# Kernel tuning notes

Hardware: AMD Instinct MI355X
Metric: run time of the kernel (lower is better)

## Reference

```python
import jax, jax.numpy as jnp
import numpy as np

ALPHA = 1.0          # gating temperature (train_alpha=False)
DEPTH = 4            # floor(log2(leaves=16))
LEAF_NUM = 16        # 2**DEPTH
N_INTERNAL = LEAF_NUM - 2  # nodes 1..14 (root handled separately)
B, D, OUT = 8192, 512, 64


def _prob(x, pw, aW, ab):
    # vectorized Node.prob with set_comps=True (comparators recomputed from batch mean)
    comp = -jnp.mean(x * pw, axis=0)                      # [in]
    dist = jax.nn.sigmoid(ALPHA * (pw * x + comp))        # [B, in]
    attn = jax.nn.softmax(x @ aW.T + ab, axis=-1)         # [B, in]
    return jnp.sum(dist * attn, axis=1, keepdims=True)    # [B, 1]


def setup_inputs() -> dict:
    key = jax.random.key(0)
    ks = jax.random.split(key, 12)
    s = 0.02
    return {
        "x": jax.random.normal(ks[0], (B, D), jnp.float32),
        # root node (input_size=D, output_size=D)
        "calc_W0": jax.random.normal(ks[1], (D, D), jnp.float32) * s,
        "calc_b0": jnp.zeros((D,), jnp.float32),
        "prob_w0": jax.random.uniform(ks[2], (D,), jnp.float32),
        "attn_W0": jax.random.normal(ks[3], (D, D), jnp.float32) * s,
        "attn_b0": jnp.zeros((D,), jnp.float32),
        # internal nodes 1..14 (input_size=2D, output_size=D), stacked
        "calc_W": jax.random.normal(ks[4], (N_INTERNAL, D, 2 * D), jnp.float32) * s,
        "calc_b": jnp.zeros((N_INTERNAL, D), jnp.float32),
        "prob_w": jax.random.uniform(ks[5], (N_INTERNAL, 2 * D), jnp.float32),
        "attn_W": jax.random.normal(ks[6], (N_INTERNAL, 2 * D, 2 * D), jnp.float32) * s,
        "attn_b": jnp.zeros((N_INTERNAL, 2 * D), jnp.float32),
        # leaf nodes: learned output vectors (torch.rand init)
        "leaf_out": jax.random.uniform(ks[7], (LEAF_NUM, OUT), jnp.float32),
    }


def reference(x, calc_W0, calc_b0, prob_w0, attn_W0, attn_b0,
              calc_W, calc_b, prob_w, attn_W, attn_b, leaf_out):
    outs, probab = {}, {}
    # root
    outs[0] = jax.nn.relu(x @ calc_W0.T + calc_b0)            # [B, D]
    p = _prob(x, prob_w0, attn_W0, attn_b0)                   # [B, 1]
    probab[1] = 1.0 - p
    probab[2] = p
    # internal nodes 1..leaf_num-2 (binary-tree routing)
    for n in range(1, LEAF_NUM - 1):
        parent = (n - 1) // 2
        inp = jnp.concatenate([outs[parent], x], axis=1)      # [B, 2D]
        outs[n] = jax.nn.relu(inp @ calc_W[n - 1].T + calc_b[n - 1])
        p = _prob(inp, prob_w[n - 1], attn_W[n - 1], attn_b[n - 1])
        probab[2 * n + 1] = probab[n] * (1.0 - p)
        probab[2 * n + 2] = probab[n] * p
    # leaves: indices LEAF_NUM-1 .. 2*LEAF_NUM-2
    leaf_p = jnp.concatenate([probab[i + LEAF_NUM - 1] for i in range(LEAF_NUM)], axis=1)  # [B, 16]
    # sum over leaves of probab * leaf_out == leaf_p @ leaf_out
    actions = leaf_p @ leaf_out                                # [B, OUT]
    return jax.nn.softmax(actions, axis=-1)
```

## Files before the change

### kernel.cpp

```cpp
#include <hip/hip_runtime.h>
#include <hip/hip_bf16.h>
#include <cstdint>


#define NROWS 8192
#define HALFD 512

typedef __bf16 bf16x8 __attribute__((ext_vector_type(8)));
typedef short  short8 __attribute__((ext_vector_type(8)));
typedef float  f32x4  __attribute__((ext_vector_type(4)));

union FragU { short8 s; bf16x8 b; };

struct GArgs {
  const __hip_bfloat16* A0[4];
  const __hip_bfloat16* Bw[4];
  const float* bias[4];
  const float* pw[4];
  const float* cm0[4];
  __hip_bfloat16* outB[4];
  float* csOut[4];
  float* S1[4];
  float* S2[4];
  int mode[4];
  int gx[4];
  int K[4];
};

__device__ __forceinline__ void gl2lds16(const void* g, void* l) {
  __builtin_amdgcn_global_load_lds((__attribute__((address_space(1))) void*)g,
                                   (__attribute__((address_space(3))) void*)l,
                                   16, 0, 0);
}

struct CvtArgs { const float* src[5]; __hip_bfloat16* dst[5]; int nblk[5]; };
__global__ void k_cvt(CvtArgs a) {
  int b = blockIdx.x, r = 0;
  while (b >= a.nblk[r]) { b -= a.nblk[r]; ++r; }
  const int i = (b * 256 + threadIdx.x) * 4;
  float4 v = *(const float4*)(a.src[r] + i);
  union { short4 s4; __hip_bfloat16 h[4]; } u;
  u.h[0] = __float2bfloat16(v.x);
  u.h[1] = __float2bfloat16(v.y);
  u.h[2] = __float2bfloat16(v.z);
  u.h[3] = __float2bfloat16(v.w);
  *(short4*)(a.dst[r] + i) = u.s4;
}

__global__ void k_colsum_f32(const float* __restrict__ src, float* __restrict__ dst) {
  int c  = blockIdx.x * 256 + threadIdx.x;
  int r0 = blockIdx.y * 256;
  float s = 0.f;
  for (int r = 0; r < 256; ++r) s += src[(size_t)(r0 + r) * HALFD + c];
  atomicAdd(&dst[c], s);
}

__global__ __launch_bounds__(256, 2)
void k_gemm(GArgs ga, const __hip_bfloat16* __restrict__ A1,
            const float* __restrict__ cm1) {
  __shared__ alignas(16) short As[128 * 64];
  __shared__ alignas(16) short Bs[128 * 64];

  const int z = blockIdx.z;
  const int id  = blockIdx.x + gridDim.x * blockIdx.y;
  const int xcd = id & 7;
  const int q   = id >> 3;
  const int bx  = q >> 3;
  const int by  = xcd * 8 + (q & 7);
  if (bx >= ga.gx[z]) return;

  const __hip_bfloat16* __restrict__ Ah0 = ga.A0[z];
  const __hip_bfloat16* __restrict__ Bw  = ga.Bw[z];
  const float* __restrict__ bias = ga.bias[z];
  const int K = ga.K[z];

  const int tid  = threadIdx.x;
  const int lane = tid & 63;
  const int wv   = tid >> 6;
  const int wm   = wv >> 1, wn = wv & 1;
  const int lr   = lane & 15, lg = lane >> 4;
  const int row0 = by * 128;
  const int col0 = bx * 128;

  f32x4 acc[4][4];
#pragma unroll
  for (int i = 0; i < 4; ++i)
#pragma unroll
    for (int j = 0; j < 4; ++j)
#pragma unroll
      for (int e = 0; e < 4; ++e) acc[i][j][e] = 0.f;

  const int sr = tid >> 3;
  const int sc = (((tid & 7) ^ (sr & 7)) << 3);
  const int sw = lr & 7;

  for (int kt = 0; kt < K; kt += 64) {
    const __hip_bfloat16* Asrc = (kt < HALFD) ? Ah0 : A1;
    const int kl = kt & (HALFD - 1);
    __syncthreads();
#pragma unroll
    for (int rnd = 0; rnd < 4; ++rnd) {
      const int r = rnd * 32 + sr;
      gl2lds16(Asrc + (size_t)(row0 + r) * HALFD + kl + sc,
               (char*)As + rnd * 4096 + wv * 1024);
      gl2lds16(Bw + (size_t)(col0 + r) * K + kt + sc,
               (char*)Bs + rnd * 4096 + wv * 1024);
    }
    __syncthreads();
#pragma unroll
    for (int kk = 0; kk < 64; kk += 32) {
      FragU a[4], b[4];
#pragma unroll
      for (int mi = 0; mi < 4; ++mi)
        a[mi].s = *(const short8*)(As + (wm * 64 + mi * 16 + lr) * 64 +
                                   ((((kk >> 3) + lg) ^ sw) << 3));
#pragma unroll
      for (int ni = 0; ni < 4; ++ni)
        b[ni].s = *(const short8*)(Bs + (wn * 64 + ni * 16 + lr) * 64 +
                                   ((((kk >> 3) + lg) ^ sw) << 3));
#pragma unroll
      for (int mi = 0; mi < 4; ++mi)
#pragma unroll
        for (int ni = 0; ni < 4; ++ni)
          acc[mi][ni] = __builtin_amdgcn_mfma_f32_16x16x32_bf16(a[mi].b, b[ni].b,
                                                               acc[mi][ni], 0, 0, 0);
    }
  }

  if (ga.mode[z] == 0) {
    __hip_bfloat16* outB = ga.outB[z];
    float* csOut = ga.csOut[z];
#pragma unroll
    for (int ni = 0; ni < 4; ++ni) {
      const int col  = col0 + wn * 64 + ni * 16 + lr;
      const float bv = bias[col];
      __hip_bfloat16* op = outB + (size_t)(col >> 9) * ((size_t)NROWS * HALFD) + (col & 511);
      float csum = 0.f;
#pragma unroll
      for (int mi = 0; mi < 4; ++mi) {
#pragma unroll
        for (int rg = 0; rg < 4; ++rg) {
          const int row = row0 + wm * 64 + mi * 16 + lg * 4 + rg;
          float v = acc[mi][ni][rg] + bv;
          v = v > 0.f ? v : 0.f;
          csum += v;
          op[(size_t)row * HALFD] = __float2bfloat16(v);
        }
      }
      csum += __shfl_xor(csum, 16);
      csum += __shfl_xor(csum, 32);
      if (lg == 0) atomicAdd(&csOut[col], csum);
    }
  } else {
    const float* __restrict__ pw  = ga.pw[z];
    const float* __restrict__ cm0 = ga.cm0[z];
    const int node  = col0 >> 10;
    const int slice = ((bx & 7) << 1) | wn;
    float* s1p = ga.S1[z] + (size_t)(node * 16 + slice) * NROWS;
    float* s2p = ga.S2[z] + (size_t)(node * 16 + slice) * NROWS;
    float bv[4], pwv[4], cmv[4];
    const __hip_bfloat16* Ain[4];
#pragma unroll
    for (int ni = 0; ni < 4; ++ni) {
      const int col = col0 + wn * 64 + ni * 16 + lr;
      bv[ni]  = bias[col];
      pwv[ni] = pw[col];
      const int ii   = col & 1023;
      const int half = ii >> 9;
      const int cc   = ii & 511;
      cmv[ni] = (half ? cm1[cc] : cm0[cc]) * (1.f / 8192.f);
      Ain[ni] = (half ? A1 : Ah0) + cc;
    }
#pragma unroll
    for (int mi = 0; mi < 4; ++mi) {
#pragma unroll
      for (int rg = 0; rg < 4; ++rg) {
        const int row = row0 + wm * 64 + mi * 16 + lg * 4 + rg;
        float s1 = 0.f, s2 = 0.f;
#pragma unroll
        for (int ni = 0; ni < 4; ++ni) {
          const float l = acc[mi][ni][rg] + bv[ni];
          const float e = __expf(l);
          const float inpv = __bfloat162float(Ain[ni][(size_t)row * HALFD]);
          const float zz = pwv[ni] * (inpv - cmv[ni]);
          const float dist = 1.f / (1.f + __expf(-zz));
          s1 += e;
          s2 += dist * e;
        }
#pragma unroll
        for (int off = 1; off < 16; off <<= 1) {
          s1 += __shfl_xor(s1, off);
          s2 += __shfl_xor(s2, off);
        }
        if (lr == 0) {
          s1p[row] = s1;
          s2p[row] = s2;
        }
      }
    }
  }
}

__global__ void k_finalize(const float* __restrict__ S1, const float* __restrict__ S2,
                           const float* __restrict__ leaf_out, float* __restrict__ out) {
  const int r    = (blockIdx.x * 256 + threadIdx.x) >> 6;
  const int lane = threadIdx.x & 63;
  float pb[31];
  pb[0] = 1.f;
#pragma unroll
  for (int n = 0; n < 15; ++n) {
    float a1 = 0.f, a2 = 0.f;
#pragma unroll
    for (int s = 0; s < 16; ++s) {
      a1 += S1[((size_t)n * 16 + s) * NROWS + r];
      a2 += S2[((size_t)n * 16 + s) * NROWS + r];
    }
    const float p = a2 / a1;
    pb[2 * n + 1] = pb[n] * (1.f - p);
    pb[2 * n + 2] = pb[n] * p;
  }
  float a = 0.f;
#pragma unroll
  for (int i = 0; i < 16; ++i) a += pb[15 + i] * leaf_out[i * 64 + lane];
  float m = a;
#pragma unroll
  for (int off = 1; off < 64; off <<= 1) m = fmaxf(m, __shfl_xor(m, off));
  const float e = __expf(a - m);
  float s = e;
#pragma unroll
  for (int off = 1; off < 64; off <<= 1) s += __shfl_xor(s, off);
  out[(size_t)r * 64 + lane] = e / s;
}

static constexpr size_t O_S1   = 0;
static constexpr size_t O_S2   = O_S1 + (size_t)15 * 16 * NROWS * 4;
static constexpr size_t O_XSUM = O_S2 + (size_t)15 * 16 * NROWS * 4;
static constexpr size_t O_CS   = O_XSUM + 512 * 4;
static constexpr size_t O_ZEND = O_CS + 7 * 512 * 4;
static constexpr size_t O_XB   = O_ZEND;
static constexpr size_t O_OUTS = O_XB + (size_t)NROWS * HALFD * 2;
static constexpr size_t O_CW0  = O_OUTS + 7 * (size_t)NROWS * HALFD * 2;
static constexpr size_t O_AW0  = O_CW0 + (size_t)512 * 512 * 2;
static constexpr size_t O_CW   = O_AW0 + (size_t)512 * 512 * 2;
static constexpr size_t O_AW   = O_CW + (size_t)14 * 512 * 1024 * 2;

extern "C" void kernel_launch(void* const* d_in, const int* in_sizes, int n_in,
                              void* d_out, int out_size, void* d_ws, size_t ws_size,
                              hipStream_t stream) {
  const float* x        = (const float*)d_in[0];
  const float* calc_b0  = (const float*)d_in[2];
  const float* prob_w0  = (const float*)d_in[3];
  const float* attn_b0  = (const float*)d_in[5];
  const float* calc_b   = (const float*)d_in[7];
  const float* prob_w   = (const float*)d_in[8];
  const float* attn_b   = (const float*)d_in[10];
  const float* leaf_out = (const float*)d_in[11];
  float* out = (float*)d_out;
  char* ws = (char*)d_ws;

  float* S1   = (float*)(ws + O_S1);
  float* S2   = (float*)(ws + O_S2);
  float* xsum = (float*)(ws + O_XSUM);
  float* cs   = (float*)(ws + O_CS);
  __hip_bfloat16* xb   = (__hip_bfloat16*)(ws + O_XB);
  __hip_bfloat16* outs = (__hip_bfloat16*)(ws + O_OUTS);
  __hip_bfloat16* cW0b = (__hip_bfloat16*)(ws + O_CW0);
  __hip_bfloat16* aW0b = (__hip_bfloat16*)(ws + O_AW0);
  __hip_bfloat16* cWb  = (__hip_bfloat16*)(ws + O_CW);
  __hip_bfloat16* aWb  = (__hip_bfloat16*)(ws + O_AW);
  const size_t OSZ = (size_t)NROWS * HALFD;
  const size_t NSL = (size_t)16 * NROWS;

  hipMemsetAsync(S1, 0, NSL * 4, stream);
  hipMemsetAsync(S2, 0, NSL * 4, stream);
  hipMemsetAsync(ws + O_XSUM, 0, O_ZEND - O_XSUM, stream);

  {
    CvtArgs ca{};
    ca.src[0] = x;                     ca.dst[0] = xb;   ca.nblk[0] = NROWS * HALFD / 1024;
    ca.src[1] = (const float*)d_in[1]; ca.dst[1] = cW0b; ca.nblk[1] = 512 * 512 / 1024;
    ca.src[2] = (const float*)d_in[4]; ca.dst[2] = aW0b; ca.nblk[2] = 512 * 512 / 1024;
    ca.src[3] = (const float*)d_in[6]; ca.dst[3] = cWb;  ca.nblk[3] = 14 * 512 * 1024 / 1024;
    ca.src[4] = (const float*)d_in[9]; ca.dst[4] = aWb;  ca.nblk[4] = 14 * 1024 * 1024 / 1024;
    int tot = ca.nblk[0] + ca.nblk[1] + ca.nblk[2] + ca.nblk[3] + ca.nblk[4];
    k_cvt<<<tot, 256, 0, stream>>>(ca);
  }
  k_colsum_f32<<<dim3(2, 32), 256, 0, stream>>>(x, xsum);

  {
    GArgs ga{};
    ga.mode[0] = 0; ga.gx[0] = 4; ga.K[0] = 512;
    ga.A0[0] = xb; ga.Bw[0] = cW0b; ga.bias[0] = calc_b0;
    ga.outB[0] = outs; ga.csOut[0] = cs;
    ga.mode[1] = 1; ga.gx[1] = 4; ga.K[1] = 512;
    ga.A0[1] = xb; ga.Bw[1] = aW0b; ga.bias[1] = attn_b0;
    ga.pw[1] = prob_w0; ga.cm0[1] = xsum;
    ga.S1[1] = S1; ga.S2[1] = S2;
    k_gemm<<<dim3(4, 64, 2), 256, 0, stream>>>(ga, xb, xsum);
  }
  {
    GArgs ga{};
    ga.mode[0] = 0; ga.gx[0] = 8; ga.K[0] = 1024;
    ga.A0[0] = outs; ga.Bw[0] = cWb; ga.bias[0] = calc_b;
    ga.outB[0] = outs + OSZ; ga.csOut[0] = cs + 512;
    ga.mode[1] = 1; ga.gx[1] = 16; ga.K[1] = 1024;
    ga.A0[1] = outs; ga.Bw[1] = aWb; ga.bias[1] = attn_b;
    ga.pw[1] = prob_w; ga.cm0[1] = cs;
    ga.S1[1] = S1 + (size_t)1 * NSL; ga.S2[1] = S2 + (size_t)1 * NSL;
    k_gemm<<<dim3(16, 64, 2), 256, 0, stream>>>(ga, xb, xsum);
  }
  {
    GArgs ga{};
    for (int i = 0; i < 2; ++i) {
      ga.mode[i] = 0; ga.gx[i] = 8; ga.K[i] = 1024;
      ga.A0[i] = outs + (size_t)(1 + i) * OSZ;
      ga.Bw[i] = cWb + (size_t)(2 + 2 * i) * 512 * 1024;
      ga.bias[i] = calc_b + (2 + 2 * i) * 512;
      ga.outB[i] = outs + (size_t)(3 + 2 * i) * OSZ;
      ga.csOut[i] = cs + (size_t)(3 + 2 * i) * 512;
    }
    for (int i = 0; i < 2; ++i) {
      const int zi = 2 + i;
      ga.mode[zi] = 1; ga.gx[zi] = 16; ga.K[zi] = 1024;
      ga.A0[zi] = outs + (size_t)(1 + i) * OSZ;
      ga.Bw[zi] = aWb + (size_t)(2 + 2 * i) * 1024 * 1024;
      ga.bias[zi] = attn_b + (2 + 2 * i) * 1024;
      ga.pw[zi] = prob_w + (2 + 2 * i) * 1024;
      ga.cm0[zi] = cs + (size_t)(1 + i) * 512;
      ga.S1[zi] = S1 + (size_t)(3 + 2 * i) * NSL;
      ga.S2[zi] = S2 + (size_t)(3 + 2 * i) * NSL;
    }
    k_gemm<<<dim3(16, 64, 4), 256, 0, stream>>>(ga, xb, xsum);
  }
  {
    GArgs ga{};
    for (int i = 0; i < 4; ++i) {
      ga.mode[i] = 1; ga.gx[i] = 16; ga.K[i] = 1024;
      ga.A0[i] = outs + (size_t)(3 + i) * OSZ;
      ga.Bw[i] = aWb + (size_t)(6 + 2 * i) * 1024 * 1024;
      ga.bias[i] = attn_b + (6 + 2 * i) * 1024;
      ga.pw[i] = prob_w + (6 + 2 * i) * 1024;
      ga.cm0[i] = cs + (size_t)(3 + i) * 512;
      ga.S1[i] = S1 + (size_t)(7 + 2 * i) * NSL;
      ga.S2[i] = S2 + (size_t)(7 + 2 * i) * NSL;
    }
    k_gemm<<<dim3(16, 64, 4), 256, 0, stream>>>(ga, xb, xsum);
  }

  k_finalize<<<NROWS * 64 / 256, 256, 0, stream>>>(S1, S2, leaf_out, out);
}
```

Measured before the change: 593.8 us.

## Double-buffer GEMM shared-memory tiles with prefetch two stages ahead

Converts the GEMM main loop to a two-buffer LDS pipeline. Tiles for steps t+1 and t+2 are issued with direct global-to-LDS loads while step t's MFMAs run, and a partial vmcnt wait replaces the full sync before each compute phase. The aim is to hide global load latency behind matrix math. In exchange LDS use per block doubles, which may cut occupancy under launch_bounds(256,2). Correctness also relies on the hardcoded vmcnt(8) matching the number of loads per stage.

New measurement: 665.3 us. +12.0%, slower.

```diff
diff --git a/kernel.cpp b/kernel.cpp
--- a/kernel.cpp
+++ b/kernel.cpp
@@ -58,8 +58,8 @@
 __global__ __launch_bounds__(256, 2)
 void k_gemm(GArgs ga, const __hip_bfloat16* __restrict__ A1,
             const float* __restrict__ cm1) {
-  __shared__ alignas(16) short As[128 * 64];
-  __shared__ alignas(16) short Bs[128 * 64];
+  __shared__ alignas(16) short As[2][128 * 64];
+  __shared__ alignas(16) short Bs[2][128 * 64];
 
   const int z = blockIdx.z;
   const int id  = blockIdx.x + gridDim.x * blockIdx.y;
@@ -72,7 +72,8 @@
   const __hip_bfloat16* __restrict__ Ah0 = ga.A0[z];
   const __hip_bfloat16* __restrict__ Bw  = ga.Bw[z];
   const float* __restrict__ bias = ga.bias[z];
-  const int K = ga.K[z];
+  const int K  = ga.K[z];
+  const int NT = K >> 6;
 
   const int tid  = threadIdx.x;
   const int lane = tid & 63;
@@ -94,29 +95,41 @@
   const int sc = (((tid & 7) ^ (sr & 7)) << 3);
   const int sw = lr & 7;
 
-  for (int kt = 0; kt < K; kt += 64) {
-    const __hip_bfloat16* Asrc = (kt < HALFD) ? Ah0 : A1;
-    const int kl = kt & (HALFD - 1);
-    __syncthreads();
+  auto STAGE = [&](int db, int tt) {
+    const __hip_bfloat16* Asrc = (tt < 8) ? Ah0 : A1;
+    const int kl = (tt & 7) << 6;
+    const int kb = tt << 6;
 #pragma unroll
     for (int rnd = 0; rnd < 4; ++rnd) {
       const int r = rnd * 32 + sr;
       gl2lds16(Asrc + (size_t)(row0 + r) * HALFD + kl + sc,
-               (char*)As + rnd * 4096 + wv * 1024);
-      gl2lds16(Bw + (size_t)(col0 + r) * K + kt + sc,
-               (char*)Bs + rnd * 4096 + wv * 1024);
-    }
-    __syncthreads();
+               (char*)As[db] + rnd * 4096 + wv * 1024);
+      gl2lds16(Bw + (size_t)(col0 + r) * K + kb + sc,
+               (char*)Bs[db] + rnd * 4096 + wv * 1024);
+    }
+  };
+
+  STAGE(0, 0);
+  STAGE(1, 1);
+
+  for (int t = 0; t < NT; ++t) {
+    if (t + 1 < NT) asm volatile("s_waitcnt vmcnt(8)" ::: "memory");
+    else            asm volatile("s_waitcnt vmcnt(0)" ::: "memory");
+    __builtin_amdgcn_s_barrier();
+    __builtin_amdgcn_sched_barrier(0);
+
+    const short* Ab = As[t & 1];
+    const short* Bb = Bs[t & 1];
 #pragma unroll
     for (int kk = 0; kk < 64; kk += 32) {
       FragU a[4], b[4];
 #pragma unroll
       for (int mi = 0; mi < 4; ++mi)
-        a[mi].s = *(const short8*)(As + (wm * 64 + mi * 16 + lr) * 64 +
+        a[mi].s = *(const short8*)(Ab + (wm * 64 + mi * 16 + lr) * 64 +
                                    ((((kk >> 3) + lg) ^ sw) << 3));
 #pragma unroll
       for (int ni = 0; ni < 4; ++ni)
-        b[ni].s = *(const short8*)(Bs + (wn * 64 + ni * 16 + lr) * 64 +
+        b[ni].s = *(const short8*)(Bb + (wn * 64 + ni * 16 + lr) * 64 +
                                    ((((kk >> 3) + lg) ^ sw) << 3));
 #pragma unroll
       for (int mi = 0; mi < 4; ++mi)
@@ -125,6 +138,10 @@
           acc[mi][ni] = __builtin_amdgcn_mfma_f32_16x16x32_bf16(a[mi].b, b[ni].b,
                                                                acc[mi][ni], 0, 0, 0);
     }
+
+    __builtin_amdgcn_sched_barrier(0);
+    __builtin_amdgcn_s_barrier();
+    if (t + 2 < NT) STAGE(t & 1, t + 2);
   }
 
   if (ga.mode[z] == 0) {
```
